# Kernel tuning notes

Hardware: AMD Instinct MI355X
Metric: run time of the kernel (lower is better)

## Reference

```python
import jax, jax.numpy as jnp
import numpy as np


def _lin(key, fin, fout):
    return jax.random.normal(key, (fin, fout), jnp.float32) / np.sqrt(fin)


def _hgt_conv(x, Wk, bk, Wq, bq, Wv, bv, a_rel, m_rel, p_rel, Wo, bo, skip, src, dst):
    # Faithful single-(node,edge)-type PyG HGTConv.
    N = x.shape[0]
    H, D = a_rel.shape[0], a_rel.shape[1]
    k = (x @ Wk + bk).reshape(N, H, D)
    q = (x @ Wq + bq).reshape(N, H, D)
    v = (x @ Wv + bv).reshape(N, H, D)
    # per-edge-type relation transforms (per-head DxD matrices)
    k = jnp.einsum('nhd,hde->nhe', k, a_rel)
    v = jnp.einsum('nhd,hde->nhe', v, m_rel)
    # attention logits per edge (j=src -> i=dst), [E,H]
    alpha = (q[dst] * k[src]).sum(-1) * p_rel / jnp.sqrt(jnp.asarray(D, x.dtype))
    # segment softmax over incoming edges of each dst node
    amax = jax.ops.segment_max(alpha, dst, num_segments=N)
    amax = jnp.where(jnp.isfinite(amax), amax, 0.0)  # empty segments
    ex = jnp.exp(alpha - amax[dst])
    denom = jax.ops.segment_sum(ex, dst, num_segments=N)
    w = ex / denom[dst]                                   # [E,H]
    agg = jax.ops.segment_sum(v[src] * w[..., None], dst, num_segments=N)
    out = jax.nn.gelu(agg.reshape(N, H * D), approximate=False) @ Wo + bo
    a = jax.nn.sigmoid(skip)  # trainable skip (in == out channels)
    return a * out + (1.0 - a) * x


def _decode(z, ei, Wlp, blp):
    src, dst = ei[0], ei[1]
    feat = jnp.concatenate([z[src], z[dst]], axis=1)
    return (feat @ Wlp + blp).squeeze(-1)


def setup_inputs() -> dict:
    N, E, P = 50000, 800000, 100000
    C, H = 128, 4
    D = C // H
    ks = jax.random.split(jax.random.key(0), 32)
    inp = {}
    inp['x'] = jax.random.normal(ks[0], (N, C), jnp.float32)
    inp['edge_index'] = jax.random.randint(ks[1], (2, E), 0, N, jnp.int32)
    inp['edge_weight'] = jax.random.uniform(ks[2], (E,), jnp.float32)
    inp['pos_edge_index'] = jax.random.randint(ks[3], (2, P), 0, N, jnp.int32)
    inp['neg_edge_index'] = jax.random.randint(ks[4], (2, P), 0, N, jnp.int32)
    i = 5
    for l in (1, 2):
        for nm in ('k', 'q', 'v'):
            inp[f'W{l}{nm}'] = _lin(ks[i], C, C); i += 1
            inp[f'b{l}{nm}'] = jnp.zeros((C,), jnp.float32)
        inp[f'a{l}'] = jax.random.normal(ks[i], (H, D, D), jnp.float32) / np.sqrt(D); i += 1
        inp[f'm{l}'] = jax.random.normal(ks[i], (H, D, D), jnp.float32) / np.sqrt(D); i += 1
        inp[f'p{l}'] = jnp.ones((H,), jnp.float32)
        inp[f'Wo{l}'] = _lin(ks[i], C, C); i += 1
        inp[f'bo{l}'] = jnp.zeros((C,), jnp.float32)
        inp[f'skip{l}'] = jnp.ones((), jnp.float32)
    inp['Wlp'] = _lin(ks[i], 2 * C, 1)
    inp['blp'] = jnp.zeros((1,), jnp.float32)
    return inp


def reference(x, edge_index, edge_weight, pos_edge_index, neg_edge_index,
              W1k, b1k, W1q, b1q, W1v, b1v, a1, m1, p1, Wo1, bo1, skip1,
              W2k, b2k, W2q, b2q, W2v, b2v, a2, m2, p2, Wo2, bo2, skip2,
              Wlp, blp):
    src, dst = edge_index[0], edge_index[1]
    h1 = _hgt_conv(x, W1k, b1k, W1q, b1q, W1v, b1v, a1, m1, p1, Wo1, bo1, skip1, src, dst)
    h2 = _hgt_conv(h1, W2k, b2k, W2q, b2q, W2v, b2v, a2, m2, p2, Wo2, bo2, skip2, src, dst)
    pos = _decode(h2, pos_edge_index, Wlp, blp)
    neg = _decode(h2, neg_edge_index, Wlp, blp)
    return (pos, neg)
```

## Files before the change

### kernel.cpp

```cpp
#include <hip/hip_runtime.h>
#include <hip/hip_bf16.h>

#define CDIV(a,b) (((a)+(b)-1)/(b))

typedef __attribute__((ext_vector_type(8))) short bh8;
typedef __attribute__((ext_vector_type(4))) float f32x4;

__device__ __forceinline__ float gelu_exact(float x){
  return 0.5f * x * (1.0f + erff(x * 0.7071067811865475f));
}
__device__ __forceinline__ float blo(unsigned u){ return __uint_as_float(u << 16); }
__device__ __forceinline__ float bhi(unsigned u){ return __uint_as_float(u & 0xFFFF0000u); }
__device__ __forceinline__ unsigned short bf16bits(float x){
  __hip_bfloat16 b = __float2bfloat16(x);
  return *(unsigned short*)&b;
}

__global__ void k_clear_int(int* __restrict__ p, int n){
  int i = blockIdx.x*256 + threadIdx.x;
  if (i < n) p[i] = 0;
}

__global__ void k_deg(const int* __restrict__ dst, int* __restrict__ deg, int E){
  int e = blockIdx.x*256 + threadIdx.x;
  if (e < E) atomicAdd(&deg[dst[e]], 1);
}

__global__ void k_scan_blk(const int* __restrict__ deg, int* __restrict__ rowp,
                           int* __restrict__ partial, int N){
  __shared__ int buf[256];
  int i = blockIdx.x*256 + threadIdx.x;
  int v = (i < N) ? deg[i] : 0;
  buf[threadIdx.x] = v;
  __syncthreads();
  #pragma unroll
  for (int off = 1; off < 256; off <<= 1){
    int t = (threadIdx.x >= off) ? buf[threadIdx.x - off] : 0;
    __syncthreads();
    buf[threadIdx.x] += t;
    __syncthreads();
  }
  if (i < N) rowp[i] = buf[threadIdx.x] - v;
  if (threadIdx.x == 255) partial[blockIdx.x] = buf[255];
}

__global__ void k_scan_mid(int* __restrict__ partial, int nb){
  __shared__ int buf[256];
  int v = (threadIdx.x < nb) ? partial[threadIdx.x] : 0;
  buf[threadIdx.x] = v;
  __syncthreads();
  #pragma unroll
  for (int off = 1; off < 256; off <<= 1){
    int t = (threadIdx.x >= off) ? buf[threadIdx.x - off] : 0;
    __syncthreads();
    buf[threadIdx.x] += t;
    __syncthreads();
  }
  if (threadIdx.x < nb) partial[threadIdx.x] = buf[threadIdx.x] - v;
}

__global__ void k_scan_add(int* __restrict__ rowp, const int* __restrict__ partial,
                           int* __restrict__ cursor, int N, int E){
  int i = blockIdx.x*256 + threadIdx.x;
  if (i < N){
    int v = rowp[i] + partial[i >> 8];
    rowp[i] = v;
    cursor[i] = v;
  }
  if (i == 0) rowp[N] = E;
}

__global__ void k_fill(const int* __restrict__ src, const int* __restrict__ dst,
                       int* __restrict__ cursor, int* __restrict__ srcs, int E){
  int e = blockIdx.x*256 + threadIdx.x;
  if (e >= E) return;
  int d = dst[e];
  int pos = atomicAdd(&cursor[d], 1);
  srcs[pos] = src[e];
}

__global__ void k_prep(const float* __restrict__ Wk, const float* __restrict__ bk,
                       const float* __restrict__ Ak, const float* __restrict__ Wq,
                       const float* __restrict__ Wv, const float* __restrict__ bv,
                       const float* __restrict__ Av, const float* __restrict__ Wo,
                       short* __restrict__ BfH,
                       float* __restrict__ beffK, float* __restrict__ beffV){
  int t = blockIdx.x*256 + threadIdx.x;
  if (t < 4*16384){
    int g = t >> 14;
    int u = t & 16383;
    int k = u & 127, n = u >> 7;
    float x;
    if (g == 1)      x = Wq[(size_t)k*128 + n];
    else if (g == 3) x = Wo[(size_t)k*128 + n];
    else {
      const float* W = (g == 0) ? Wk : Wv;
      const float* A = (g == 0) ? Ak : Av;
      int h = n >> 5, e2 = n & 31;
      const float* s  = W + (size_t)k*128 + h*32;
      const float* Ah = A + h*1024 + e2;
      float acc = 0.f;
      #pragma unroll
      for (int d = 0; d < 32; ++d) acc += s[d] * Ah[d*32];
      x = acc;
    }
    int nt = n >> 4, lr = n & 15, ks = k >> 5, lk = (k >> 3) & 3, e = k & 7;
    size_t o = ((size_t)((g*8 + nt)*4 + ks)*64 + lr*4 + lk)*8 + e;
    BfH[o] = (short)bf16bits(x);
  } else {
    int u = t - 4*16384;
    if (u < 256){
      int which = u >> 7, n = u & 127;
      const float* b = which ? bv : bk;
      const float* A = which ? Av : Ak;
      int h = n >> 5, e2 = n & 31;
      const float* Ah = A + h*1024 + e2;
      float acc = 0.f;
      #pragma unroll
      for (int d = 0; d < 32; ++d) acc += b[h*32 + d] * Ah[d*32];
      (which ? beffV : beffK)[n] = acc;
    }
  }
}

__global__ __launch_bounds__(256)
void k_kqv(const float* __restrict__ A,
           const short* __restrict__ BfH,
           const float* __restrict__ bK, const float* __restrict__ bQ,
           const float* __restrict__ bV,
           unsigned short* __restrict__ KV16, unsigned short* __restrict__ Qb16, int M){
  const int tid = threadIdx.x;
  const int wm = tid >> 6, l = tid & 63;
  const int lr = l & 15, lk = l >> 4;
  const int perm = (lr*4 + lk)*8;
  const int p0 = blockIdx.x*8 + wm*2;

  bh8 a_h[2][4], a_l[2][4];
  #pragma unroll
  for (int p = 0; p < 2; ++p){
    int row = (p0 + p)*16 + lr;
    #pragma unroll
    for (int ks = 0; ks < 4; ++ks){
      float f[8] = {0.f,0.f,0.f,0.f,0.f,0.f,0.f,0.f};
      if (row < M){
        float4 va = *(const float4*)(A + (size_t)row*128 + ks*32 + lk*8);
        float4 vb = *(const float4*)(A + (size_t)row*128 + ks*32 + lk*8 + 4);
        f[0]=va.x; f[1]=va.y; f[2]=va.z; f[3]=va.w;
        f[4]=vb.x; f[5]=vb.y; f[6]=vb.z; f[7]=vb.w;
      }
      bh8 h8, l8;
      #pragma unroll
      for (int q = 0; q < 8; ++q){
        unsigned ub = __float_as_uint(f[q]);
        h8[q] = (short)(ub >> 16);
        float fhv = __uint_as_float(ub & 0xFFFF0000u);
        l8[q] = (short)(__float_as_uint(f[q] - fhv) >> 16);
      }
      a_h[p][ks] = h8;
      a_l[p][ks] = l8;
    }
  }

  #pragma unroll
  for (int g = 0; g < 3; ++g){
    f32x4 acc[2][8];
    #pragma unroll
    for (int p = 0; p < 2; ++p)
      #pragma unroll
      for (int i = 0; i < 8; ++i) acc[p][i] = (f32x4){0.f,0.f,0.f,0.f};
    #pragma unroll
    for (int ks = 0; ks < 4; ++ks){
      #pragma unroll
      for (int nt = 0; nt < 8; ++nt){
        size_t o = (size_t)((g*8 + nt)*4 + ks)*512 + perm;
        bh8 bh_ = *(const bh8*)(BfH + o);
        #pragma unroll
        for (int p = 0; p < 2; ++p){
          acc[p][nt] = __builtin_amdgcn_mfma_f32_16x16x32_bf16(bh_, a_h[p][ks], acc[p][nt], 0, 0, 0);
          acc[p][nt] = __builtin_amdgcn_mfma_f32_16x16x32_bf16(bh_, a_l[p][ks], acc[p][nt], 0, 0, 0);
        }
      }
    }
    const float* bias = (g==0) ? bK : (g==1) ? bQ : bV;
    #pragma unroll
    for (int p = 0; p < 2; ++p){
      int r = (p0 + p)*16 + lr;
      if (r >= M) continue;
      #pragma unroll
      for (int nt = 0; nt < 8; ++nt){
        int c0 = nt*16 + lk*4;
        float4 bs = *(const float4*)(bias + c0);
        float v0 = acc[p][nt][0] + bs.x;
        float v1 = acc[p][nt][1] + bs.y;
        float v2 = acc[p][nt][2] + bs.z;
        float v3 = acc[p][nt][3] + bs.w;
        unsigned u0 = (unsigned)bf16bits(v0) | ((unsigned)bf16bits(v1) << 16);
        unsigned u1 = (unsigned)bf16bits(v2) | ((unsigned)bf16bits(v3) << 16);
        if (g == 1){
          *(uint2*)(Qb16 + (size_t)r*128 + c0) = make_uint2(u0, u1);
        } else {
          *(uint2*)(KV16 + (size_t)r*256 + (size_t)(nt*4 + lk)*8 + ((g == 2) ? 4 : 0))
              = make_uint2(u0, u1);
        }
      }
    }
  }
}

__global__ __launch_bounds__(256)
void k_outgemm(const short* __restrict__ AfH, const short* __restrict__ AfL,
               const short* __restrict__ BfH,
               const float* __restrict__ bias, const float* __restrict__ mixsrc,
               const float* __restrict__ skipp, float* __restrict__ out, int M){
  const int tid = threadIdx.x;
  const int wm = tid >> 6, l = tid & 63;
  const int lr = l & 15, lk = l >> 4;
  const int perm = (lr*4 + lk)*8;
  const int p0 = blockIdx.x*8 + wm*2;

  bh8 a_h[2][4], a_l[2][4];
  #pragma unroll
  for (int p = 0; p < 2; ++p)
    #pragma unroll
    for (int ks = 0; ks < 4; ++ks){
      size_t o = (size_t)((p0 + p)*4 + ks)*512 + perm;
      a_h[p][ks] = *(const bh8*)(AfH + o);
      a_l[p][ks] = *(const bh8*)(AfL + o);
    }

  f32x4 acc[2][8];
  #pragma unroll
  for (int p = 0; p < 2; ++p)
    #pragma unroll
    for (int i = 0; i < 8; ++i) acc[p][i] = (f32x4){0.f,0.f,0.f,0.f};
  #pragma unroll
  for (int ks = 0; ks < 4; ++ks){
    #pragma unroll
    for (int nt = 0; nt < 8; ++nt){
      size_t o = (size_t)((3*8 + nt)*4 + ks)*512 + perm;
      bh8 bh_ = *(const bh8*)(BfH + o);
      #pragma unroll
      for (int p = 0; p < 2; ++p){
        acc[p][nt] = __builtin_amdgcn_mfma_f32_16x16x32_bf16(bh_, a_h[p][ks], acc[p][nt], 0, 0, 0);
        acc[p][nt] = __builtin_amdgcn_mfma_f32_16x16x32_bf16(bh_, a_l[p][ks], acc[p][nt], 0, 0, 0);
      }
    }
  }
  float sg = 1.f / (1.f + expf(-skipp[0]));
  #pragma unroll
  for (int p = 0; p < 2; ++p){
    int r = (p0 + p)*16 + lr;
    if (r >= M) continue;
    #pragma unroll
    for (int nt = 0; nt < 8; ++nt){
      int c0 = nt*16 + lk*4;
      float4 bs  = *(const float4*)(bias + c0);
      float4 mx  = *(const float4*)(mixsrc + (size_t)r*128 + c0);
      float4 o4;
      o4.x = sg*(acc[p][nt][0] + bs.x) + (1.f - sg)*mx.x;
      o4.y = sg*(acc[p][nt][1] + bs.y) + (1.f - sg)*mx.y;
      o4.z = sg*(acc[p][nt][2] + bs.z) + (1.f - sg)*mx.z;
      o4.w = sg*(acc[p][nt][3] + bs.w) + (1.f - sg)*mx.w;
      *(float4*)(out + (size_t)r*128 + c0) = o4;
    }
  }
}

__global__ __launch_bounds__(256)
void k_node(const unsigned short* __restrict__ KV, const unsigned short* __restrict__ Qb,
            const int* __restrict__ srcs, const int* __restrict__ row_ptr,
            const float* __restrict__ p,
            short* __restrict__ fh, short* __restrict__ fl, int NN){
  int wave = threadIdx.x >> 6;
  int lane = threadIdx.x & 63;
  int L = lane & 31;
  int node = blockIdx.x*8 + wave*2 + (lane >> 5);
  if (node >= NN) return;
  int start = row_ptr[node], end = row_ptr[node+1];
  int h = L >> 3;
  float ph = p[h] * 0.25504366769049834f;
  const unsigned short* KVl = KV + L*8;
  uint2 qu = *(const uint2*)(Qb + (size_t)node*128 + L*4);
  float4 qv = make_float4(blo(qu.x), bhi(qu.x), blo(qu.y), bhi(qu.y));

  float a0=0.f, a1=0.f, a2=0.f, a3=0.f, den=0.f;
  int j = start;
  for (; j + 3 < end; j += 4){
    int s0 = srcs[j], s1 = srcs[j+1], s2 = srcs[j+2], s3 = srcs[j+3];
    uint4 kv0 = *(const uint4*)(KVl + (size_t)s0*256);
    uint4 kv1 = *(const uint4*)(KVl + (size_t)s1*256);
    uint4 kv2 = *(const uint4*)(KVl + (size_t)s2*256);
    uint4 kv3 = *(const uint4*)(KVl + (size_t)s3*256);
    float d0 = blo(kv0.x)*qv.x + bhi(kv0.x)*qv.y + blo(kv0.y)*qv.z + bhi(kv0.y)*qv.w;
    float d1 = blo(kv1.x)*qv.x + bhi(kv1.x)*qv.y + blo(kv1.y)*qv.z + bhi(kv1.y)*qv.w;
    float d2 = blo(kv2.x)*qv.x + bhi(kv2.x)*qv.y + blo(kv2.y)*qv.z + bhi(kv2.y)*qv.w;
    float d3 = blo(kv3.x)*qv.x + bhi(kv3.x)*qv.y + blo(kv3.y)*qv.z + bhi(kv3.y)*qv.w;
    #pragma unroll
    for (int m = 1; m < 8; m <<= 1){
      d0 += __shfl_xor(d0, m);
      d1 += __shfl_xor(d1, m);
      d2 += __shfl_xor(d2, m);
      d3 += __shfl_xor(d3, m);
    }
    float w0 = exp2f(d0 * ph);
    float w1 = exp2f(d1 * ph);
    float w2 = exp2f(d2 * ph);
    float w3 = exp2f(d3 * ph);
    den += (w0 + w1) + (w2 + w3);
    a0 += (w0*blo(kv0.z) + w1*blo(kv1.z)) + (w2*blo(kv2.z) + w3*blo(kv3.z));
    a1 += (w0*bhi(kv0.z) + w1*bhi(kv1.z)) + (w2*bhi(kv2.z) + w3*bhi(kv3.z));
    a2 += (w0*blo(kv0.w) + w1*blo(kv1.w)) + (w2*blo(kv2.w) + w3*blo(kv3.w));
    a3 += (w0*bhi(kv0.w) + w1*bhi(kv1.w)) + (w2*bhi(kv2.w) + w3*bhi(kv3.w));
  }
  for (; j < end; ++j){
    int s0 = srcs[j];
    uint4 kv0 = *(const uint4*)(KVl + (size_t)s0*256);
    float d0 = blo(kv0.x)*qv.x + bhi(kv0.x)*qv.y + blo(kv0.y)*qv.z + bhi(kv0.y)*qv.w;
    #pragma unroll
    for (int m = 1; m < 8; m <<= 1) d0 += __shfl_xor(d0, m);
    float w0 = exp2f(d0 * ph);
    den += w0;
    a0 += w0*blo(kv0.z);
    a1 += w0*bhi(kv0.z);
    a2 += w0*blo(kv0.w);
    a3 += w0*bhi(kv0.w);
  }
  float o[4] = {0.f, 0.f, 0.f, 0.f};
  if (end > start){
    float inv = 1.f / den;
    o[0] = gelu_exact(a0 * inv);
    o[1] = gelu_exact(a1 * inv);
    o[2] = gelu_exact(a2 * inv);
    o[3] = gelu_exact(a3 * inv);
  }
  unsigned hh[4], ll[4];
  #pragma unroll
  for (int q = 0; q < 4; ++q){
    unsigned ub = __float_as_uint(o[q]);
    hh[q] = ub >> 16;
    ll[q] = __float_as_uint(o[q] - __uint_as_float(ub & 0xFFFF0000u)) >> 16;
  }
  size_t ci = (size_t)((node >> 4)*4 + h)*64 + (node & 15)*4 + ((L >> 1) & 3);
  size_t si = ci*8 + (L & 1)*4;
  uint2 uh = make_uint2(hh[0] | (hh[1] << 16), hh[2] | (hh[3] << 16));
  uint2 ul = make_uint2(ll[0] | (ll[1] << 16), ll[2] | (ll[3] << 16));
  *(uint2*)(fh + si) = uh;
  *(uint2*)(fl + si) = ul;
}

__global__ void k_gemv2(const float* __restrict__ z, const float* __restrict__ Wlp,
                        float* __restrict__ s1, float* __restrict__ s2, int NN){
  int n = blockIdx.x*256 + threadIdx.x;
  if (n >= NN) return;
  const float4* row = (const float4*)(z + (size_t)n*128);
  float a0 = 0.f, a1 = 0.f;
  #pragma unroll
  for (int i = 0; i < 32; ++i){
    float4 v  = row[i];
    float4 w1 = ((const float4*)Wlp)[i];
    float4 w2 = ((const float4*)Wlp)[32 + i];
    a0 += v.x*w1.x + v.y*w1.y + v.z*w1.z + v.w*w1.w;
    a1 += v.x*w2.x + v.y*w2.y + v.z*w2.z + v.w*w2.w;
  }
  s1[n] = a0; s2[n] = a1;
}

__global__ void k_decode(const int* __restrict__ pe, const int* __restrict__ ne,
                         const float* __restrict__ s1, const float* __restrict__ s2,
                         const float* __restrict__ blp, float* __restrict__ out, int P){
  int i = blockIdx.x*256 + threadIdx.x;
  if (i < P){
    out[i] = s1[pe[i]] + s2[pe[P + i]] + blp[0];
  } else if (i < 2*P){
    int j = i - P;
    out[P + j] = s1[ne[j]] + s2[ne[P + j]] + blp[0];
  }
}

extern "C" void kernel_launch(void* const* d_in, const int* in_sizes, int n_in,
                              void* d_out, int out_size, void* d_ws, size_t ws_size,
                              hipStream_t stream){
  const float* x      = (const float*)d_in[0];
  const int*   ei     = (const int*)d_in[1];
  const int*   pos_ei = (const int*)d_in[3];
  const int*   neg_ei = (const int*)d_in[4];
  const int NN = in_sizes[0] / 128;
  const int E  = in_sizes[1] / 2;
  const int P  = in_sizes[3] / 2;
  const int padM = CDIV(NN, 128) * 128;
  const int* e_src = ei;
  const int* e_dst = ei + E;

  char* wsb = (char*)d_ws;
  size_t off = 0;
  auto alloc = [&](size_t bytes)->char*{
    char* r = wsb + off;
    off = (off + bytes + 255) & ~(size_t)255;
    return r;
  };
  unsigned short* KV16 = (unsigned short*)alloc((size_t)NN*256*2);
  unsigned short* Qb16 = (unsigned short*)alloc((size_t)NN*128*2);
  float* h1     = (float*)alloc((size_t)NN*128*4);
  float* h2     = (float*)alloc((size_t)NN*128*4);
  short* AfH    = (short*)alloc((size_t)padM*128*2);
  short* AfL    = (short*)alloc((size_t)padM*128*2);
  int*   srcs   = (int*)alloc((size_t)E*4);
  int*   rowp   = (int*)alloc((size_t)(NN+1)*4);
  int*   deg    = (int*)alloc((size_t)NN*4);
  int*   cursor = (int*)alloc((size_t)NN*4);
  int*   partial= (int*)alloc(256*4);
  float* beffK1 = (float*)alloc(128*4);
  float* beffV1 = (float*)alloc(128*4);
  float* beffK2 = (float*)alloc(128*4);
  float* beffV2 = (float*)alloc(128*4);
  short* BfH1   = (short*)alloc((size_t)4*16384*2);
  short* BfH2   = (short*)alloc((size_t)4*16384*2);
  float* s1     = (float*)alloc((size_t)NN*4);
  float* s2     = (float*)alloc((size_t)NN*4);

  const int nb = CDIV(NN, 256);
  k_clear_int<<<CDIV(NN,256),256,0,stream>>>(deg, NN);
  k_deg<<<CDIV(E,256),256,0,stream>>>(e_dst, deg, E);
  k_scan_blk<<<nb,256,0,stream>>>(deg, rowp, partial, NN);
  k_scan_mid<<<1,256,0,stream>>>(partial, nb);
  k_scan_add<<<CDIV(NN,256),256,0,stream>>>(rowp, partial, cursor, NN, E);
  k_fill<<<CDIV(E,256),256,0,stream>>>(e_src, e_dst, cursor, srcs, E);
  k_prep<<<CDIV(4*16384+256,256),256,0,stream>>>(
      (const float*)d_in[5],  (const float*)d_in[6],  (const float*)d_in[11],
      (const float*)d_in[7],  (const float*)d_in[9],  (const float*)d_in[10],
      (const float*)d_in[12], (const float*)d_in[14],
      BfH1, beffK1, beffV1);
  k_prep<<<CDIV(4*16384+256,256),256,0,stream>>>(
      (const float*)d_in[17], (const float*)d_in[18], (const float*)d_in[23],
      (const float*)d_in[19], (const float*)d_in[21], (const float*)d_in[22],
      (const float*)d_in[24], (const float*)d_in[26],
      BfH2, beffK2, beffV2);

  const int gblk = padM / 128;
  auto layer = [&](const float* hin, float* hout, int base,
                   const short* BfH, const float* beffK, const float* beffV){
    const float* bq  = (const float*)d_in[base+3];
    const float* p   = (const float*)d_in[base+8];
    const float* bo  = (const float*)d_in[base+10];
    const float* sk  = (const float*)d_in[base+11];
    k_kqv<<<gblk,256,0,stream>>>(hin, BfH, beffK, bq, beffV, KV16, Qb16, NN);
    k_node<<<CDIV(NN,8),256,0,stream>>>(KV16, Qb16, srcs, rowp, p, AfH, AfL, NN);
    k_outgemm<<<gblk,256,0,stream>>>(AfH, AfL, BfH, bo, hin, sk, hout, NN);
  };
  layer(x,  h1, 5,  BfH1, beffK1, beffV1);
  layer(h1, h2, 17, BfH2, beffK2, beffV2);

  k_gemv2<<<CDIV(NN,256),256,0,stream>>>(h2, (const float*)d_in[29], s1, s2, NN);
  k_decode<<<CDIV(2*P,256),256,0,stream>>>(pos_ei, neg_ei, s1, s2,
                                           (const float*)d_in[30], (float*)d_out, P);
}
```

Measured before the change: 328.1 us.

## Drop bf16 split-precision for aggregated features, fuse decode GEMV and scan passes

The aggregated attention output is now stored as a single bf16 value instead of a hi/lo bf16 pair, which halves the A-operand loads and MFMAs in the output GEMM and removes one store stream from the node kernel. The second layer's output GEMM computes the two link-prediction dot products directly and no longer writes h2, which removes the separate GEMV kernel and a full N×128 float round trip. The mid and add scan kernels are merged into one kernel in which each block reduces the preceding partial sums itself. Dropping the low half lowers the precision of the GEMM input, which may affect accuracy tolerance.

```diff
diff --git a/kernel.cpp b/kernel.cpp
--- a/kernel.cpp
+++ b/kernel.cpp
@@ -44,28 +44,21 @@
   if (threadIdx.x == 255) partial[blockIdx.x] = buf[255];
 }
 
-__global__ void k_scan_mid(int* __restrict__ partial, int nb){
-  __shared__ int buf[256];
-  int v = (threadIdx.x < nb) ? partial[threadIdx.x] : 0;
-  buf[threadIdx.x] = v;
+__global__ void k_scan_fin(int* __restrict__ rowp, const int* __restrict__ partial,
+                           int* __restrict__ cursor, int N, int E, int nb){
+  __shared__ int ws[4];
+  int t = threadIdx.x;
+  int v = (t < nb && t < blockIdx.x) ? partial[t] : 0;
+  #pragma unroll
+  for (int m = 32; m; m >>= 1) v += __shfl_xor(v, m);
+  if ((t & 63) == 0) ws[t >> 6] = v;
   __syncthreads();
-  #pragma unroll
-  for (int off = 1; off < 256; off <<= 1){
-    int t = (threadIdx.x >= off) ? buf[threadIdx.x - off] : 0;
-    __syncthreads();
-    buf[threadIdx.x] += t;
-    __syncthreads();
-  }
-  if (threadIdx.x < nb) partial[threadIdx.x] = buf[threadIdx.x] - v;
-}
-
-__global__ void k_scan_add(int* __restrict__ rowp, const int* __restrict__ partial,
-                           int* __restrict__ cursor, int N, int E){
-  int i = blockIdx.x*256 + threadIdx.x;
+  int pre = ws[0] + ws[1] + ws[2] + ws[3];
+  int i = blockIdx.x*256 + t;
   if (i < N){
-    int v = rowp[i] + partial[i >> 8];
-    rowp[i] = v;
-    cursor[i] = v;
+    int nv = rowp[i] + pre;
+    rowp[i] = nv;
+    cursor[i] = nv;
   }
   if (i == 0) rowp[N] = E;
 }
@@ -207,25 +200,27 @@
   }
 }
 
+template<bool DECODE>
 __global__ __launch_bounds__(256)
-void k_outgemm(const short* __restrict__ AfH, const short* __restrict__ AfL,
+void k_outgemm(const short* __restrict__ AfH,
                const short* __restrict__ BfH,
                const float* __restrict__ bias, const float* __restrict__ mixsrc,
-               const float* __restrict__ skipp, float* __restrict__ out, int M){
+               const float* __restrict__ skipp, float* __restrict__ out,
+               const float* __restrict__ Wlp,
+               float* __restrict__ s1, float* __restrict__ s2, int M){
   const int tid = threadIdx.x;
   const int wm = tid >> 6, l = tid & 63;
   const int lr = l & 15, lk = l >> 4;
   const int perm = (lr*4 + lk)*8;
   const int p0 = blockIdx.x*8 + wm*2;
 
-  bh8 a_h[2][4], a_l[2][4];
+  bh8 a_h[2][4];
   #pragma unroll
   for (int p = 0; p < 2; ++p)
     #pragma unroll
     for (int ks = 0; ks < 4; ++ks){
       size_t o = (size_t)((p0 + p)*4 + ks)*512 + perm;
       a_h[p][ks] = *(const bh8*)(AfH + o);
-      a_l[p][ks] = *(const bh8*)(AfL + o);
     }
 
   f32x4 acc[2][8];
@@ -242,7 +237,6 @@
       #pragma unroll
       for (int p = 0; p < 2; ++p){
         acc[p][nt] = __builtin_amdgcn_mfma_f32_16x16x32_bf16(bh_, a_h[p][ks], acc[p][nt], 0, 0, 0);
-        acc[p][nt] = __builtin_amdgcn_mfma_f32_16x16x32_bf16(bh_, a_l[p][ks], acc[p][nt], 0, 0, 0);
       }
     }
   }
@@ -251,6 +245,7 @@
   for (int p = 0; p < 2; ++p){
     int r = (p0 + p)*16 + lr;
     if (r >= M) continue;
+    float d1 = 0.f, d2 = 0.f;
     #pragma unroll
     for (int nt = 0; nt < 8; ++nt){
       int c0 = nt*16 + lk*4;
@@ -261,7 +256,19 @@
       o4.y = sg*(acc[p][nt][1] + bs.y) + (1.f - sg)*mx.y;
       o4.z = sg*(acc[p][nt][2] + bs.z) + (1.f - sg)*mx.z;
       o4.w = sg*(acc[p][nt][3] + bs.w) + (1.f - sg)*mx.w;
-      *(float4*)(out + (size_t)r*128 + c0) = o4;
+      if (DECODE){
+        float4 w1 = *(const float4*)(Wlp + c0);
+        float4 w2 = *(const float4*)(Wlp + 128 + c0);
+        d1 += o4.x*w1.x + o4.y*w1.y + o4.z*w1.z + o4.w*w1.w;
+        d2 += o4.x*w2.x + o4.y*w2.y + o4.z*w2.z + o4.w*w2.w;
+      } else {
+        *(float4*)(out + (size_t)r*128 + c0) = o4;
+      }
+    }
+    if (DECODE){
+      d1 += __shfl_xor(d1, 16); d1 += __shfl_xor(d1, 32);
+      d2 += __shfl_xor(d2, 16); d2 += __shfl_xor(d2, 32);
+      if (lk == 0){ s1[r] = d1; s2[r] = d2; }
     }
   }
 }
@@ -270,7 +277,7 @@
 void k_node(const unsigned short* __restrict__ KV, const unsigned short* __restrict__ Qb,
             const int* __restrict__ srcs, const int* __restrict__ row_ptr,
             const float* __restrict__ p,
-            short* __restrict__ fh, short* __restrict__ fl, int NN){
+            short* __restrict__ fh, int NN){
   int wave = threadIdx.x >> 6;
   int lane = threadIdx.x & 63;
   int L = lane & 31;
@@ -333,36 +340,11 @@
     o[2] = gelu_exact(a2 * inv);
     o[3] = gelu_exact(a3 * inv);
   }
-  unsigned hh[4], ll[4];
-  #pragma unroll
-  for (int q = 0; q < 4; ++q){
-    unsigned ub = __float_as_uint(o[q]);
-    hh[q] = ub >> 16;
-    ll[q] = __float_as_uint(o[q] - __uint_as_float(ub & 0xFFFF0000u)) >> 16;
-  }
   size_t ci = (size_t)((node >> 4)*4 + h)*64 + (node & 15)*4 + ((L >> 1) & 3);
   size_t si = ci*8 + (L & 1)*4;
-  uint2 uh = make_uint2(hh[0] | (hh[1] << 16), hh[2] | (hh[3] << 16));
-  uint2 ul = make_uint2(ll[0] | (ll[1] << 16), ll[2] | (ll[3] << 16));
+  uint2 uh = make_uint2((unsigned)bf16bits(o[0]) | ((unsigned)bf16bits(o[1]) << 16),
+                        (unsigned)bf16bits(o[2]) | ((unsigned)bf16bits(o[3]) << 16));
   *(uint2*)(fh + si) = uh;
-  *(uint2*)(fl + si) = ul;
-}
-
-__global__ void k_gemv2(const float* __restrict__ z, const float* __restrict__ Wlp,
-                        float* __restrict__ s1, float* __restrict__ s2, int NN){
-  int n = blockIdx.x*256 + threadIdx.x;
-  if (n >= NN) return;
-  const float4* row = (const float4*)(z + (size_t)n*128);
-  float a0 = 0.f, a1 = 0.f;
-  #pragma unroll
-  for (int i = 0; i < 32; ++i){
-    float4 v  = row[i];
-    float4 w1 = ((const float4*)Wlp)[i];
-    float4 w2 = ((const float4*)Wlp)[32 + i];
-    a0 += v.x*w1.x + v.y*w1.y + v.z*w1.z + v.w*w1.w;
-    a1 += v.x*w2.x + v.y*w2.y + v.z*w2.z + v.w*w2.w;
-  }
-  s1[n] = a0; s2[n] = a1;
 }
 
 __global__ void k_decode(const int* __restrict__ pe, const int* __restrict__ ne,
@@ -401,9 +383,7 @@
   unsigned short* KV16 = (unsigned short*)alloc((size_t)NN*256*2);
   unsigned short* Qb16 = (unsigned short*)alloc((size_t)NN*128*2);
   float* h1     = (float*)alloc((size_t)NN*128*4);
-  float* h2     = (float*)alloc((size_t)NN*128*4);
   short* AfH    = (short*)alloc((size_t)padM*128*2);
-  short* AfL    = (short*)alloc((size_t)padM*128*2);
   int*   srcs   = (int*)alloc((size_t)E*4);
   int*   rowp   = (int*)alloc((size_t)(NN+1)*4);
   int*   deg    = (int*)alloc((size_t)NN*4);
@@ -422,8 +402,7 @@
   k_clear_int<<<CDIV(NN,256),256,0,stream>>>(deg, NN);
   k_deg<<<CDIV(E,256),256,0,stream>>>(e_dst, deg, E);
   k_scan_blk<<<nb,256,0,stream>>>(deg, rowp, partial, NN);
-  k_scan_mid<<<1,256,0,stream>>>(partial, nb);
-  k_scan_add<<<CDIV(NN,256),256,0,stream>>>(rowp, partial, cursor, NN, E);
+  k_scan_fin<<<nb,256,0,stream>>>(rowp, partial, cursor, NN, E, nb);
   k_fill<<<CDIV(E,256),256,0,stream>>>(e_src, e_dst, cursor, srcs, E);
   k_prep<<<CDIV(4*16384+256,256),256,0,stream>>>(
       (const float*)d_in[5],  (const float*)d_in[6],  (const float*)d_in[11],
@@ -437,20 +416,23 @@
       BfH2, beffK2, beffV2);
 
   const int gblk = padM / 128;
-  auto layer = [&](const float* hin, float* hout, int base,
-                   const short* BfH, const float* beffK, const float* beffV){
-    const float* bq  = (const float*)d_in[base+3];
-    const float* p   = (const float*)d_in[base+8];
-    const float* bo  = (const float*)d_in[base+10];
-    const float* sk  = (const float*)d_in[base+11];
-    k_kqv<<<gblk,256,0,stream>>>(hin, BfH, beffK, bq, beffV, KV16, Qb16, NN);
-    k_node<<<CDIV(NN,8),256,0,stream>>>(KV16, Qb16, srcs, rowp, p, AfH, AfL, NN);
-    k_outgemm<<<gblk,256,0,stream>>>(AfH, AfL, BfH, bo, hin, sk, hout, NN);
-  };
-  layer(x,  h1, 5,  BfH1, beffK1, beffV1);
-  layer(h1, h2, 17, BfH2, beffK2, beffV2);
-
-  k_gemv2<<<CDIV(NN,256),256,0,stream>>>(h2, (const float*)d_in[29], s1, s2, NN);
+  const float* Wlp = (const float*)d_in[29];
+
+  k_kqv<<<gblk,256,0,stream>>>(x, BfH1, beffK1, (const float*)d_in[8], beffV1,
+                               KV16, Qb16, NN);
+  k_node<<<CDIV(NN,8),256,0,stream>>>(KV16, Qb16, srcs, rowp,
+                                      (const float*)d_in[13], AfH, NN);
+  k_outgemm<false><<<gblk,256,0,stream>>>(AfH, BfH1, (const float*)d_in[15], x,
+                                          (const float*)d_in[16], h1,
+                                          nullptr, nullptr, nullptr, NN);
+  k_kqv<<<gblk,256,0,stream>>>(h1, BfH2, beffK2, (const float*)d_in[20], beffV2,
+                               KV16, Qb16, NN);
+  k_node<<<CDIV(NN,8),256,0,stream>>>(KV16, Qb16, srcs, rowp,
+                                      (const float*)d_in[25], AfH, NN);
+  k_outgemm<true><<<gblk,256,0,stream>>>(AfH, BfH2, (const float*)d_in[27], h1,
+                                         (const float*)d_in[28], nullptr,
+                                         Wlp, s1, s2, NN);
+
   k_decode<<<CDIV(2*P,256),256,0,stream>>>(pos_ei, neg_ei, s1, s2,
                                            (const float*)d_in[30], (float*)d_out, P);
 }
```

After: 306.9 us. 6.5% less time.
